# Kernel tuning notes

Measured on AMD Instinct MI355X. Metric: run time of the kernel, lower is better.

The kernel has to match this reference:

```python
import jax, jax.numpy as jnp
import numpy as np

N_NODES = 100000
N_EDGES = 3200000
FEAT = 128
HID = 128
N_GRAPHS = 512


def setup_inputs() -> dict:
    key = jax.random.key(0)
    ks = jax.random.split(key, 16)
    x = jax.random.normal(ks[0], (N_NODES, FEAT), dtype=jnp.float32)
    edge_index = jax.random.randint(ks[1], (2, N_EDGES), 0, N_NODES, dtype=jnp.int32)
    edge_weight = jax.random.uniform(ks[2], (N_EDGES,), dtype=jnp.float32)
    batch = jnp.sort(jax.random.randint(ks[3], (N_NODES,), 0, N_GRAPHS, dtype=jnp.int32))
    s = 1.0 / np.sqrt(HID)
    W1 = jax.random.uniform(ks[4], (FEAT, HID), dtype=jnp.float32, minval=-s, maxval=s)
    W2 = jax.random.uniform(ks[5], (HID, HID), dtype=jnp.float32, minval=-s, maxval=s)
    W3 = jax.random.uniform(ks[6], (HID, HID), dtype=jnp.float32, minval=-s, maxval=s)
    W4 = jax.random.uniform(ks[7], (HID, HID), dtype=jnp.float32, minval=-s, maxval=s)
    b1 = jnp.zeros((HID,), jnp.float32)
    b2 = jnp.zeros((HID,), jnp.float32)
    b3 = jnp.zeros((HID,), jnp.float32)
    b4 = jnp.zeros((HID,), jnp.float32)
    Wc = jax.random.uniform(ks[8], (HID, 1), dtype=jnp.float32, minval=-s, maxval=s)
    bc = jnp.zeros((1,), jnp.float32)
    return dict(x=x, edge_index=edge_index, edge_weight=edge_weight, batch=batch,
                W1=W1, b1=b1, W2=W2, b2=b2, W3=W3, b3=b3, W4=W4, b4=b4, Wc=Wc, bc=bc)


def _gcn_norm(edge_index, edge_weight, n):
    # PyG gcn_norm with add_self_loops=True (self-loop weight 1)
    loop = jnp.arange(n, dtype=edge_index.dtype)
    src = jnp.concatenate([edge_index[0], loop])
    dst = jnp.concatenate([edge_index[1], loop])
    ew = jnp.concatenate([edge_weight, jnp.ones((n,), edge_weight.dtype)])
    deg = jax.ops.segment_sum(ew, dst, num_segments=n)
    dinv = jnp.where(deg > 0, jax.lax.rsqrt(jnp.maximum(deg, 1e-30)), 0.0)
    norm = dinv[src] * ew * dinv[dst]
    return src, dst, norm


def _gcn_conv(x, src, dst, norm, W, b, n):
    h = x @ W                      # [N, H] dense GEMM
    msg = h[src] * norm[:, None]   # [E+N, H] gather + scale
    out = jax.ops.segment_sum(msg, dst, num_segments=n)  # scatter-add
    return out + b


def reference(x, edge_index, edge_weight, batch,
              W1, b1, W2, b2, W3, b3, W4, b4, Wc, bc):
    n = x.shape[0]
    src, dst, norm = _gcn_norm(edge_index, edge_weight, n)
    h = jax.nn.relu(_gcn_conv(x, src, dst, norm, W1, b1, n))
    h = jax.nn.relu(_gcn_conv(h, src, dst, norm, W2, b2, n))
    h = jax.nn.relu(_gcn_conv(h, src, dst, norm, W3, b3, n))
    h = jax.nn.relu(_gcn_conv(h, src, dst, norm, W4, b4, n))
    # global mean pool over graphs
    sums = jax.ops.segment_sum(h, batch, num_segments=N_GRAPHS)
    cnt = jax.ops.segment_sum(jnp.ones((n,), h.dtype), batch, num_segments=N_GRAPHS)
    pooled = sums / jnp.maximum(cnt, 1.0)[:, None]
    return jax.nn.sigmoid(pooled @ Wc + bc)
```

## Files before the change

### kernel.cpp

```cpp
#include <hip/hip_runtime.h>
#include <math.h>


#define MASK40 ((1ull << 40) - 1)

typedef float v2f __attribute__((ext_vector_type(2)));
typedef __bf16 bf16x8 __attribute__((ext_vector_type(8)));
typedef float f32x4 __attribute__((ext_vector_type(4)));

__device__ inline unsigned f2bf(float x) {
    unsigned u = __float_as_uint(x);
    return (u + 0x7FFFu + ((u >> 16) & 1u)) >> 16;
}

__global__ void init_packed(unsigned long long* packed, int n) {
    int i = blockIdx.x * blockDim.x + threadIdx.x;
    if (i < n) packed[i] = 0ull;
}

__global__ void edge_pass(const int* __restrict__ dst, const float* __restrict__ ew,
                          unsigned long long* packed, unsigned short* __restrict__ slot,
                          int E) {
    int e = blockIdx.x * blockDim.x + threadIdx.x;
    if (e < E) {
        int d = dst[e];
        unsigned int fx = (unsigned int)rintf(ew[e] * 16777216.0f);
        unsigned long long old =
            atomicAdd(&packed[d], (1ull << 40) | (unsigned long long)fx);
        slot[e] = (unsigned short)(old >> 40);
    }
}

__global__ void dinv_cnt_k(const unsigned long long* __restrict__ packed,
                           float* dinv, int* cnt, int n) {
    int i = blockIdx.x * blockDim.x + threadIdx.x;
    if (i < n) {
        unsigned long long p = packed[i];
        float deg = 1.0f + (float)(p & MASK40) * (1.0f / 16777216.0f);
        dinv[i] = rsqrtf(deg);
        cnt[i] = (int)(p >> 40);
    }
}

__global__ __launch_bounds__(1024) void scan1(const int* __restrict__ cnt, int* rowp,
                                              int* bsums, int total, int N) {
    __shared__ int sh[1024];
    int i = blockIdx.x * 1024 + threadIdx.x;
    int v = 0;
    if (i < N) v = cnt[i] + 1;
    sh[threadIdx.x] = v;
    __syncthreads();
    for (int off = 1; off < 1024; off <<= 1) {
        int t = (threadIdx.x >= (unsigned)off) ? sh[threadIdx.x - off] : 0;
        __syncthreads();
        sh[threadIdx.x] += t;
        __syncthreads();
    }
    if (i < total) rowp[i] = sh[threadIdx.x] - v;
    if (threadIdx.x == 1023) bsums[blockIdx.x] = sh[1023];
}

__global__ void scan2(int* bsums, int nb) {
    if (threadIdx.x == 0 && blockIdx.x == 0) {
        int run = 0;
        for (int b = 0; b < nb; ++b) { int t = bsums[b]; bsums[b] = run; run += t; }
    }
}

__global__ __launch_bounds__(1024) void scan3(int* rowp, const int* __restrict__ bsums,
                                              int total) {
    int i = blockIdx.x * 1024 + threadIdx.x;
    if (i < total) rowp[i] += bsums[blockIdx.x];
}

__global__ void selfloop_k(const int* __restrict__ rowp, const float* __restrict__ dinv,
                           int2* colval, int n) {
    int i = blockIdx.x * blockDim.x + threadIdx.x;
    if (i < n) {
        float dv = dinv[i];
        int2 cv;
        cv.x = i;
        cv.y = __float_as_int(dv * dv);
        colval[rowp[i]] = cv;
    }
}

__global__ void scatter2(const int* __restrict__ src, const int* __restrict__ dst,
                         const float* __restrict__ ew,
                         const unsigned short* __restrict__ slot,
                         const float* __restrict__ dinv, const int* __restrict__ rowp,
                         int2* colval, int E) {
    int e = blockIdx.x * blockDim.x + threadIdx.x;
    if (e < E) {
        int s = src[e], d = dst[e];
        int idx = rowp[d] + 1 + (int)slot[e];
        int2 cv;
        cv.x = s;
        cv.y = __float_as_int(dinv[s] * ew[e] * dinv[d]);
        colval[idx] = cv;
    }
}

__global__ void cvt_x(const float2* __restrict__ x, unsigned* __restrict__ xb,
                      long n64) {
    long t = (long)blockIdx.x * 256 + threadIdx.x;
    if (t < n64) {
        float2 f = x[t];
        xb[t] = f2bf(f.x) | (f2bf(f.y) << 16);
    }
}

__global__ void prep_w(const float* __restrict__ Wa, const float* __restrict__ Wb,
                       const float* __restrict__ Wc, const float* __restrict__ Wd,
                       unsigned short* __restrict__ Wt) {
    const int l = blockIdx.y;
    const float* W = (l == 0) ? Wa : (l == 1) ? Wb : (l == 2) ? Wc : Wd;
    const int c = blockIdx.x, p = threadIdx.x;
    int k;
    if (l == 0) {
        k = p;
    } else {
        int t = p >> 1, h = p & 1;
        int i = t >> 2, s = (t >> 1) & 1, jj = 2 * (t & 1) + h;
        k = 16 * (4 * s + jj) + i;
    }
    float v = W[k * 128 + c];
    unsigned u = __float_as_uint(v);
    Wt[l * 16384 + c * 128 + p] = (unsigned short)((u + 0x7FFFu + ((u >> 16) & 1u)) >> 16);
}

__global__ __launch_bounds__(256) void gemm_mfma(const uint4* __restrict__ A,
                                                 const uint4* __restrict__ Wt,
                                                 uint2* __restrict__ C) {
    const int w = threadIdx.x >> 6;
    const int lane = threadIdx.x & 63;
    const int i = lane & 15, q = lane >> 4;
    const long row_base = (long)blockIdx.x * 64 + w * 16;

    f32x4 acc[8];
#pragma unroll
    for (int t = 0; t < 8; ++t) acc[t] = (f32x4){0.f, 0.f, 0.f, 0.f};

    const uint4* Arow = A + (row_base + i) * 16 + q;
#pragma unroll
    for (int ks = 0; ks < 4; ++ks) {
        const bf16x8 af = __builtin_bit_cast(bf16x8, Arow[ks * 4]);
#pragma unroll
        for (int ct = 0; ct < 8; ++ct) {
            const bf16x8 bf = __builtin_bit_cast(
                bf16x8, Wt[(size_t)(ct * 16 + i) * 16 + ks * 4 + q]);
            acc[ct] = __builtin_amdgcn_mfma_f32_16x16x32_bf16(af, bf, acc[ct], 0, 0, 0);
        }
    }

#pragma unroll
    for (int reg = 0; reg < 4; ++reg) {
        int d0 = __builtin_amdgcn_cvt_pk_fp8_f32(acc[0][reg], acc[1][reg], 0, false);
        d0     = __builtin_amdgcn_cvt_pk_fp8_f32(acc[2][reg], acc[3][reg], d0, true);
        int d1 = __builtin_amdgcn_cvt_pk_fp8_f32(acc[4][reg], acc[5][reg], 0, false);
        d1     = __builtin_amdgcn_cvt_pk_fp8_f32(acc[6][reg], acc[7][reg], d1, true);
        const long row = row_base + q * 4 + reg;
        uint2 o; o.x = (unsigned)d0; o.y = (unsigned)d1;
        C[row * 16 + i] = o;
    }
}

__device__ inline int perm_f0(int lane) {
    return 64 * ((lane >> 1) & 1) + 32 * (lane & 1) + (lane >> 2);
}

__global__ __launch_bounds__(64) void aggregate(const unsigned short* __restrict__ t8,
                                                const int* __restrict__ rowp,
                                                const int2* __restrict__ colval,
                                                const float* __restrict__ bias,
                                                unsigned* __restrict__ out16, int n) {
    const int v = blockIdx.x;
    const int lane = threadIdx.x;
    const int e0 = rowp[v], e1 = rowp[v + 1];
    float ax = 0.f, ay = 0.f;
    int e = e0;
    for (; e + 4 <= e1; e += 4) {
        const int2 cv0 = colval[e],     cv1 = colval[e + 1];
        const int2 cv2 = colval[e + 2], cv3 = colval[e + 3];
        const unsigned short u0 = t8[(size_t)cv0.x * 64 + lane];
        const unsigned short u1 = t8[(size_t)cv1.x * 64 + lane];
        const unsigned short u2 = t8[(size_t)cv2.x * 64 + lane];
        const unsigned short u3 = t8[(size_t)cv3.x * 64 + lane];
        const float w0 = __int_as_float(cv0.y), w1 = __int_as_float(cv1.y);
        const float w2 = __int_as_float(cv2.y), w3 = __int_as_float(cv3.y);
        const v2f h0 = __builtin_amdgcn_cvt_pk_f32_fp8((int)u0, false);
        const v2f h1 = __builtin_amdgcn_cvt_pk_f32_fp8((int)u1, false);
        const v2f h2 = __builtin_amdgcn_cvt_pk_f32_fp8((int)u2, false);
        const v2f h3 = __builtin_amdgcn_cvt_pk_f32_fp8((int)u3, false);
        ax = fmaf(w0, h0.x, ax); ay = fmaf(w0, h0.y, ay);
        ax = fmaf(w1, h1.x, ax); ay = fmaf(w1, h1.y, ay);
        ax = fmaf(w2, h2.x, ax); ay = fmaf(w2, h2.y, ay);
        ax = fmaf(w3, h3.x, ax); ay = fmaf(w3, h3.y, ay);
    }
    for (; e < e1; ++e) {
        const int2 cv = colval[e];
        const v2f hv = __builtin_amdgcn_cvt_pk_f32_fp8(
            (int)t8[(size_t)cv.x * 64 + lane], false);
        const float w = __int_as_float(cv.y);
        ax = fmaf(w, hv.x, ax); ay = fmaf(w, hv.y, ay);
    }
    const int f0 = perm_f0(lane);
    const float rx = fmaxf(ax + bias[f0], 0.f);
    const float ry = fmaxf(ay + bias[f0 + 16], 0.f);
    out16[(size_t)v * 64 + lane] = f2bf(rx) | (f2bf(ry) << 16);
}

__global__ __launch_bounds__(64) void aggregate_last(const unsigned short* __restrict__ t8,
                                                     const int* __restrict__ rowp,
                                                     const int2* __restrict__ colval,
                                                     const float* __restrict__ bias,
                                                     const float* __restrict__ Wc,
                                                     float* __restrict__ sv, int n) {
    const int v = blockIdx.x;
    const int lane = threadIdx.x;
    const int e0 = rowp[v], e1 = rowp[v + 1];
    float ax = 0.f, ay = 0.f;
    int e = e0;
    for (; e + 4 <= e1; e += 4) {
        const int2 cv0 = colval[e],     cv1 = colval[e + 1];
        const int2 cv2 = colval[e + 2], cv3 = colval[e + 3];
        const unsigned short u0 = t8[(size_t)cv0.x * 64 + lane];
        const unsigned short u1 = t8[(size_t)cv1.x * 64 + lane];
        const unsigned short u2 = t8[(size_t)cv2.x * 64 + lane];
        const unsigned short u3 = t8[(size_t)cv3.x * 64 + lane];
        const float w0 = __int_as_float(cv0.y), w1 = __int_as_float(cv1.y);
        const float w2 = __int_as_float(cv2.y), w3 = __int_as_float(cv3.y);
        const v2f h0 = __builtin_amdgcn_cvt_pk_f32_fp8((int)u0, false);
        const v2f h1 = __builtin_amdgcn_cvt_pk_f32_fp8((int)u1, false);
        const v2f h2 = __builtin_amdgcn_cvt_pk_f32_fp8((int)u2, false);
        const v2f h3 = __builtin_amdgcn_cvt_pk_f32_fp8((int)u3, false);
        ax = fmaf(w0, h0.x, ax); ay = fmaf(w0, h0.y, ay);
        ax = fmaf(w1, h1.x, ax); ay = fmaf(w1, h1.y, ay);
        ax = fmaf(w2, h2.x, ax); ay = fmaf(w2, h2.y, ay);
        ax = fmaf(w3, h3.x, ax); ay = fmaf(w3, h3.y, ay);
    }
    for (; e < e1; ++e) {
        const int2 cv = colval[e];
        const v2f hv = __builtin_amdgcn_cvt_pk_f32_fp8(
            (int)t8[(size_t)cv.x * 64 + lane], false);
        const float w = __int_as_float(cv.y);
        ax = fmaf(w, hv.x, ax); ay = fmaf(w, hv.y, ay);
    }
    const int f0 = perm_f0(lane);
    float p = fmaxf(ax + bias[f0], 0.f) * Wc[f0] +
              fmaxf(ay + bias[f0 + 16], 0.f) * Wc[f0 + 16];
#pragma unroll
    for (int off = 32; off; off >>= 1) p += __shfl_down(p, off);
    if (lane == 0) sv[v] = p;
}

__global__ void gstart_k(const int* __restrict__ batch, int* start, int N, int G) {
    int g = blockIdx.x * blockDim.x + threadIdx.x;
    if (g <= G) {
        int lo = 0, hi = N;
        while (lo < hi) {
            int mid = (lo + hi) >> 1;
            if (batch[mid] < g) lo = mid + 1; else hi = mid;
        }
        start[g] = lo;
    }
}

__global__ __launch_bounds__(256) void seg_pool(const float* __restrict__ sv,
                                                const int* __restrict__ start,
                                                const float* __restrict__ bc,
                                                float* __restrict__ out, int G) {
    __shared__ float sh[4];
    const int g = blockIdx.x;
    const int s = start[g], epos = start[g + 1];
    float acc = 0.f;
    for (int i = s + threadIdx.x; i < epos; i += 256) acc += sv[i];
#pragma unroll
    for (int off = 32; off; off >>= 1) acc += __shfl_down(acc, off);
    if ((threadIdx.x & 63) == 0) sh[threadIdx.x >> 6] = acc;
    __syncthreads();
    if (threadIdx.x == 0) {
        float sum = sh[0] + sh[1] + sh[2] + sh[3];
        float cnt = (float)(epos - s);
        float z = sum / fmaxf(cnt, 1.0f) + bc[0];
        out[g] = 1.0f / (1.0f + expf(-z));
    }
}

extern "C" void kernel_launch(void* const* d_in, const int* in_sizes, int n_in,
                              void* d_out, int out_size, void* d_ws, size_t ws_size,
                              hipStream_t stream) {
    const float* x   = (const float*)d_in[0];
    const int* ei    = (const int*)d_in[1];
    const float* ew  = (const float*)d_in[2];
    const int* batch = (const int*)d_in[3];
    const float* W1 = (const float*)d_in[4];  const float* b1 = (const float*)d_in[5];
    const float* W2 = (const float*)d_in[6];  const float* b2 = (const float*)d_in[7];
    const float* W3 = (const float*)d_in[8];  const float* b3 = (const float*)d_in[9];
    const float* W4 = (const float*)d_in[10]; const float* b4 = (const float*)d_in[11];
    const float* Wc = (const float*)d_in[12]; const float* bc = (const float*)d_in[13];

    const int N = in_sizes[0] / 128;
    const int E = in_sizes[2];
    const int G = out_size;
    const int* src = ei;
    const int* dst = ei + E;
    const int nblk = (N + 63) / 64;
    const long Npad = (long)nblk * 64;

    char* p = (char*)d_ws;
    auto alloc = [&](size_t bytes) {
        void* q = (void*)p;
        p += (bytes + 255) & ~(size_t)255;
        return q;
    };
    unsigned long long* packed = (unsigned long long*)alloc((size_t)N * 8);
    float* dinv = (float*)alloc((size_t)N * 4);
    int* cnt    = (int*)alloc((size_t)N * 4);
    unsigned short* slot = (unsigned short*)alloc((size_t)E * 2);
    int* rowp   = (int*)alloc((size_t)(N + 1) * 4);
    int* bsums  = (int*)alloc(1024 * 4);
    const size_t M = (size_t)E + (size_t)N;
    int2* colval = (int2*)alloc(M * 8);
    unsigned* tbuf = (unsigned*)alloc((size_t)Npad * 32 * 4);
    unsigned* hbuf = (unsigned*)alloc((size_t)Npad * 64 * 4);
    unsigned* xb   = (unsigned*)alloc((size_t)Npad * 64 * 4);
    unsigned short* Wt = (unsigned short*)alloc(4 * 16384 * 2);
    float* sv   = (float*)alloc((size_t)N * 4);
    int* start  = (int*)alloc((size_t)(G + 1) * 4);

    const int B = 256;
    init_packed<<<(N + B - 1) / B, B, 0, stream>>>(packed, N);
    edge_pass<<<(E + B - 1) / B, B, 0, stream>>>(dst, ew, packed, slot, E);
    dinv_cnt_k<<<(N + B - 1) / B, B, 0, stream>>>(packed, dinv, cnt, N);
    const int total = N + 1;
    const int nb = (total + 1023) / 1024;
    scan1<<<nb, 1024, 0, stream>>>(cnt, rowp, bsums, total, N);
    scan2<<<1, 64, 0, stream>>>(bsums, nb);
    scan3<<<nb, 1024, 0, stream>>>(rowp, bsums, total);
    selfloop_k<<<(N + B - 1) / B, B, 0, stream>>>(rowp, dinv, colval, N);
    scatter2<<<(E + B - 1) / B, B, 0, stream>>>(src, dst, ew, slot, dinv, rowp,
                                                colval, E);
    gstart_k<<<(G + 1 + B - 1) / B, B, 0, stream>>>(batch, start, N, G);

    const long n64 = (long)N * 64;
    cvt_x<<<(int)((n64 + 255) / 256), B, 0, stream>>>((const float2*)x, xb, n64);
    prep_w<<<dim3(128, 4), 128, 0, stream>>>(W1, W2, W3, W4, Wt);

    const unsigned short* t8 = (const unsigned short*)tbuf;
    const uint4* Wt4 = (const uint4*)Wt;
    gemm_mfma<<<nblk, B, 0, stream>>>((const uint4*)xb,   Wt4,         (uint2*)tbuf);
    aggregate<<<N, 64, 0, stream>>>(t8, rowp, colval, b1, hbuf, N);
    gemm_mfma<<<nblk, B, 0, stream>>>((const uint4*)hbuf, Wt4 + 2048,  (uint2*)tbuf);
    aggregate<<<N, 64, 0, stream>>>(t8, rowp, colval, b2, hbuf, N);
    gemm_mfma<<<nblk, B, 0, stream>>>((const uint4*)hbuf, Wt4 + 4096,  (uint2*)tbuf);
    aggregate<<<N, 64, 0, stream>>>(t8, rowp, colval, b3, hbuf, N);
    gemm_mfma<<<nblk, B, 0, stream>>>((const uint4*)hbuf, Wt4 + 6144,  (uint2*)tbuf);
    aggregate_last<<<N, 64, 0, stream>>>(t8, rowp, colval, b4, Wc, sv, N);

    seg_pool<<<G, B, 0, stream>>>(sv, start, bc, (float*)d_out, G);
}
```

Baseline: 859.9 us.

## Quantize GEMM outputs to FP4 with per-row scale and fuse input conversion

```diff
diff --git a/kernel.cpp b/kernel.cpp
--- a/kernel.cpp
+++ b/kernel.cpp
@@ -4,13 +4,18 @@
 
 #define MASK40 ((1ull << 40) - 1)
 
-typedef float v2f __attribute__((ext_vector_type(2)));
 typedef __bf16 bf16x8 __attribute__((ext_vector_type(8)));
 typedef float f32x4 __attribute__((ext_vector_type(4)));
 
 __device__ inline unsigned f2bf(float x) {
     unsigned u = __float_as_uint(x);
     return (u + 0x7FFFu + ((u >> 16) & 1u)) >> 16;
+}
+
+__device__ inline unsigned fp4_bf16(unsigned nib) {
+    unsigned n = nib & 7u, s = (nib >> 3) << 15;
+    unsigned t10 = (n == 0) ? 0u : (0xFCu + n - (n == 1 ? 1u : 0u));
+    return (t10 << 6) | s;
 }
 
 __global__ void init_packed(unsigned long long* packed, int n) {
@@ -31,23 +36,18 @@
     }
 }
 
-__global__ void dinv_cnt_k(const unsigned long long* __restrict__ packed,
-                           float* dinv, int* cnt, int n) {
-    int i = blockIdx.x * blockDim.x + threadIdx.x;
-    if (i < n) {
-        unsigned long long p = packed[i];
-        float deg = 1.0f + (float)(p & MASK40) * (1.0f / 16777216.0f);
-        dinv[i] = rsqrtf(deg);
-        cnt[i] = (int)(p >> 40);
-    }
-}
-
-__global__ __launch_bounds__(1024) void scan1(const int* __restrict__ cnt, int* rowp,
+__global__ __launch_bounds__(1024) void scan1(const unsigned long long* __restrict__ packed,
+                                              float* __restrict__ dinv, int* rowp,
                                               int* bsums, int total, int N) {
     __shared__ int sh[1024];
     int i = blockIdx.x * 1024 + threadIdx.x;
     int v = 0;
-    if (i < N) v = cnt[i] + 1;
+    if (i < N) {
+        unsigned long long p = packed[i];
+        float deg = 1.0f + (float)(p & MASK40) * (1.0f / 16777216.0f);
+        dinv[i] = rsqrtf(deg);
+        v = (int)(p >> 40) + 1;
+    }
     sh[threadIdx.x] = v;
     __syncthreads();
     for (int off = 1; off < 1024; off <<= 1) {
@@ -101,15 +101,6 @@
     }
 }
 
-__global__ void cvt_x(const float2* __restrict__ x, unsigned* __restrict__ xb,
-                      long n64) {
-    long t = (long)blockIdx.x * 256 + threadIdx.x;
-    if (t < n64) {
-        float2 f = x[t];
-        xb[t] = f2bf(f.x) | (f2bf(f.y) << 16);
-    }
-}
-
 __global__ void prep_w(const float* __restrict__ Wa, const float* __restrict__ Wb,
                        const float* __restrict__ Wc, const float* __restrict__ Wd,
                        unsigned short* __restrict__ Wt) {
@@ -117,92 +108,127 @@
     const float* W = (l == 0) ? Wa : (l == 1) ? Wb : (l == 2) ? Wc : Wd;
     const int c = blockIdx.x, p = threadIdx.x;
     int k;
-    if (l == 0) {
-        k = p;
-    } else {
-        int t = p >> 1, h = p & 1;
-        int i = t >> 2, s = (t >> 1) & 1, jj = 2 * (t & 1) + h;
-        k = 16 * (4 * s + jj) + i;
-    }
+    if (l == 0) k = p;
+    else       k = 32 * ((p >> 1) & 3) + (p >> 3) + 16 * (p & 1);
     float v = W[k * 128 + c];
     unsigned u = __float_as_uint(v);
     Wt[l * 16384 + c * 128 + p] = (unsigned short)((u + 0x7FFFu + ((u >> 16) & 1u)) >> 16);
 }
 
-__global__ __launch_bounds__(256) void gemm_mfma(const uint4* __restrict__ A,
+template <int FP32IN>
+__global__ __launch_bounds__(256) void gemm_mfma(const void* __restrict__ Av,
                                                  const uint4* __restrict__ Wt,
-                                                 uint2* __restrict__ C) {
+                                                 unsigned* __restrict__ C4,
+                                                 float* __restrict__ sc, int N) {
     const int w = threadIdx.x >> 6;
     const int lane = threadIdx.x & 63;
-    const int i = lane & 15, q = lane >> 4;
+    const int li = lane & 15, q = lane >> 4;
     const long row_base = (long)blockIdx.x * 64 + w * 16;
+    const long arow = (row_base + li < (long)N) ? row_base + li : (long)N - 1;
 
     f32x4 acc[8];
 #pragma unroll
     for (int t = 0; t < 8; ++t) acc[t] = (f32x4){0.f, 0.f, 0.f, 0.f};
 
-    const uint4* Arow = A + (row_base + i) * 16 + q;
 #pragma unroll
     for (int ks = 0; ks < 4; ++ks) {
-        const bf16x8 af = __builtin_bit_cast(bf16x8, Arow[ks * 4]);
+        bf16x8 af;
+        if (FP32IN) {
+            const float* Ar = (const float*)Av + arow * 128 + ks * 32 + q * 8;
+            const float4 fa = *(const float4*)Ar;
+            const float4 fb = *(const float4*)(Ar + 4);
+            unsigned p0 = f2bf(fa.x) | (f2bf(fa.y) << 16);
+            unsigned p1 = f2bf(fa.z) | (f2bf(fa.w) << 16);
+            unsigned p2 = f2bf(fb.x) | (f2bf(fb.y) << 16);
+            unsigned p3 = f2bf(fb.z) | (f2bf(fb.w) << 16);
+            uint4 u; u.x = p0; u.y = p1; u.z = p2; u.w = p3;
+            af = __builtin_bit_cast(bf16x8, u);
+        } else {
+            af = __builtin_bit_cast(bf16x8,
+                ((const uint4*)Av)[arow * 16 + ks * 4 + q]);
+        }
 #pragma unroll
         for (int ct = 0; ct < 8; ++ct) {
             const bf16x8 bf = __builtin_bit_cast(
-                bf16x8, Wt[(size_t)(ct * 16 + i) * 16 + ks * 4 + q]);
+                bf16x8, Wt[(size_t)(ct * 16 + li) * 16 + ks * 4 + q]);
             acc[ct] = __builtin_amdgcn_mfma_f32_16x16x32_bf16(af, bf, acc[ct], 0, 0, 0);
         }
     }
 
 #pragma unroll
     for (int reg = 0; reg < 4; ++reg) {
-        int d0 = __builtin_amdgcn_cvt_pk_fp8_f32(acc[0][reg], acc[1][reg], 0, false);
-        d0     = __builtin_amdgcn_cvt_pk_fp8_f32(acc[2][reg], acc[3][reg], d0, true);
-        int d1 = __builtin_amdgcn_cvt_pk_fp8_f32(acc[4][reg], acc[5][reg], 0, false);
-        d1     = __builtin_amdgcn_cvt_pk_fp8_f32(acc[6][reg], acc[7][reg], d1, true);
+        float amax = 0.f;
+#pragma unroll
+        for (int ct = 0; ct < 8; ++ct) amax = fmaxf(amax, fabsf(acc[ct][reg]));
+#pragma unroll
+        for (int m = 1; m < 16; m <<= 1) amax = fmaxf(amax, __shfl_xor(amax, m));
+        const float inv = (amax > 0.f) ? 6.0f / amax : 0.f;
         const long row = row_base + q * 4 + reg;
-        uint2 o; o.x = (unsigned)d0; o.y = (unsigned)d1;
-        C[row * 16 + i] = o;
+        if (li == 0) sc[row] = amax * (1.0f / 6.0f);
+        unsigned u = 0;
+#pragma unroll
+        for (int ct = 0; ct < 8; ++ct) {
+            const float y = acc[ct][reg] * inv;
+            const float a = fabsf(y);
+            unsigned n = (unsigned)(a >= 0.25f) + (unsigned)(a >= 0.75f)
+                       + (unsigned)(a >= 1.25f) + (unsigned)(a >= 1.75f)
+                       + (unsigned)(a >= 2.5f)  + (unsigned)(a >= 3.5f)
+                       + (unsigned)(a >= 5.0f);
+            n |= (y < 0.f) ? 8u : 0u;
+            u |= n << (ct * 4);
+        }
+        C4[row * 16 + li] = u;
     }
 }
 
 __device__ inline int perm_f0(int lane) {
-    return 64 * ((lane >> 1) & 1) + 32 * (lane & 1) + (lane >> 2);
-}
-
-__global__ __launch_bounds__(64) void aggregate(const unsigned short* __restrict__ t8,
+    return 32 * (lane & 3) + (lane >> 2);
+}
+
+__global__ __launch_bounds__(64) void aggregate(const unsigned char* __restrict__ t4,
+                                                const float* __restrict__ sc,
                                                 const int* __restrict__ rowp,
                                                 const int2* __restrict__ colval,
                                                 const float* __restrict__ bias,
                                                 unsigned* __restrict__ out16, int n) {
+    __shared__ unsigned lut[256];
     const int v = blockIdx.x;
     const int lane = threadIdx.x;
+    for (int j = lane; j < 256; j += 64)
+        lut[j] = fp4_bf16(j & 15) | (fp4_bf16(j >> 4) << 16);
+    __syncthreads();
+
     const int e0 = rowp[v], e1 = rowp[v + 1];
     float ax = 0.f, ay = 0.f;
     int e = e0;
     for (; e + 4 <= e1; e += 4) {
         const int2 cv0 = colval[e],     cv1 = colval[e + 1];
         const int2 cv2 = colval[e + 2], cv3 = colval[e + 3];
-        const unsigned short u0 = t8[(size_t)cv0.x * 64 + lane];
-        const unsigned short u1 = t8[(size_t)cv1.x * 64 + lane];
-        const unsigned short u2 = t8[(size_t)cv2.x * 64 + lane];
-        const unsigned short u3 = t8[(size_t)cv3.x * 64 + lane];
-        const float w0 = __int_as_float(cv0.y), w1 = __int_as_float(cv1.y);
-        const float w2 = __int_as_float(cv2.y), w3 = __int_as_float(cv3.y);
-        const v2f h0 = __builtin_amdgcn_cvt_pk_f32_fp8((int)u0, false);
-        const v2f h1 = __builtin_amdgcn_cvt_pk_f32_fp8((int)u1, false);
-        const v2f h2 = __builtin_amdgcn_cvt_pk_f32_fp8((int)u2, false);
-        const v2f h3 = __builtin_amdgcn_cvt_pk_f32_fp8((int)u3, false);
-        ax = fmaf(w0, h0.x, ax); ay = fmaf(w0, h0.y, ay);
-        ax = fmaf(w1, h1.x, ax); ay = fmaf(w1, h1.y, ay);
-        ax = fmaf(w2, h2.x, ax); ay = fmaf(w2, h2.y, ay);
-        ax = fmaf(w3, h3.x, ax); ay = fmaf(w3, h3.y, ay);
+        const unsigned b0 = t4[(size_t)cv0.x * 64 + lane];
+        const unsigned b1 = t4[(size_t)cv1.x * 64 + lane];
+        const unsigned b2 = t4[(size_t)cv2.x * 64 + lane];
+        const unsigned b3 = t4[(size_t)cv3.x * 64 + lane];
+        const float w0 = __int_as_float(cv0.y) * sc[cv0.x];
+        const float w1 = __int_as_float(cv1.y) * sc[cv1.x];
+        const float w2 = __int_as_float(cv2.y) * sc[cv2.x];
+        const float w3 = __int_as_float(cv3.y) * sc[cv3.x];
+        const unsigned u0 = lut[b0], u1 = lut[b1], u2 = lut[b2], u3 = lut[b3];
+        ax = fmaf(w0, __uint_as_float(u0 << 16), ax);
+        ay = fmaf(w0, __uint_as_float(u0 & 0xFFFF0000u), ay);
+        ax = fmaf(w1, __uint_as_float(u1 << 16), ax);
+        ay = fmaf(w1, __uint_as_float(u1 & 0xFFFF0000u), ay);
+        ax = fmaf(w2, __uint_as_float(u2 << 16), ax);
+        ay = fmaf(w2, __uint_as_float(u2 & 0xFFFF0000u), ay);
+        ax = fmaf(w3, __uint_as_float(u3 << 16), ax);
+        ay = fmaf(w3, __uint_as_float(u3 & 0xFFFF0000u), ay);
     }
     for (; e < e1; ++e) {
         const int2 cv = colval[e];
-        const v2f hv = __builtin_amdgcn_cvt_pk_f32_fp8(
-            (int)t8[(size_t)cv.x * 64 + lane], false);
-        const float w = __int_as_float(cv.y);
-        ax = fmaf(w, hv.x, ax); ay = fmaf(w, hv.y, ay);
+        const unsigned b = t4[(size_t)cv.x * 64 + lane];
+        const float w = __int_as_float(cv.y) * sc[cv.x];
+        const unsigned u = lut[b];
+        ax = fmaf(w, __uint_as_float(u << 16), ax);
+        ay = fmaf(w, __uint_as_float(u & 0xFFFF0000u), ay);
     }
     const int f0 = perm_f0(lane);
     const float rx = fmaxf(ax + bias[f0], 0.f);
@@ -210,41 +236,51 @@
     out16[(size_t)v * 64 + lane] = f2bf(rx) | (f2bf(ry) << 16);
 }
 
-__global__ __launch_bounds__(64) void aggregate_last(const unsigned short* __restrict__ t8,
+__global__ __launch_bounds__(64) void aggregate_last(const unsigned char* __restrict__ t4,
+                                                     const float* __restrict__ sc,
                                                      const int* __restrict__ rowp,
                                                      const int2* __restrict__ colval,
                                                      const float* __restrict__ bias,
                                                      const float* __restrict__ Wc,
                                                      float* __restrict__ sv, int n) {
+    __shared__ unsigned lut[256];
     const int v = blockIdx.x;
     const int lane = threadIdx.x;
+    for (int j = lane; j < 256; j += 64)
+        lut[j] = fp4_bf16(j & 15) | (fp4_bf16(j >> 4) << 16);
+    __syncthreads();
+
     const int e0 = rowp[v], e1 = rowp[v + 1];
     float ax = 0.f, ay = 0.f;
     int e = e0;
     for (; e + 4 <= e1; e += 4) {
         const int2 cv0 = colval[e],     cv1 = colval[e + 1];
         const int2 cv2 = colval[e + 2], cv3 = colval[e + 3];
-        const unsigned short u0 = t8[(size_t)cv0.x * 64 + lane];
-        const unsigned short u1 = t8[(size_t)cv1.x * 64 + lane];
-        const unsigned short u2 = t8[(size_t)cv2.x * 64 + lane];
-        const unsigned short u3 = t8[(size_t)cv3.x * 64 + lane];
-        const float w0 = __int_as_float(cv0.y), w1 = __int_as_float(cv1.y);
-        const float w2 = __int_as_float(cv2.y), w3 = __int_as_float(cv3.y);
-        const v2f h0 = __builtin_amdgcn_cvt_pk_f32_fp8((int)u0, false);
-        const v2f h1 = __builtin_amdgcn_cvt_pk_f32_fp8((int)u1, false);
-        const v2f h2 = __builtin_amdgcn_cvt_pk_f32_fp8((int)u2, false);
-        const v2f h3 = __builtin_amdgcn_cvt_pk_f32_fp8((int)u3, false);
-        ax = fmaf(w0, h0.x, ax); ay = fmaf(w0, h0.y, ay);
-        ax = fmaf(w1, h1.x, ax); ay = fmaf(w1, h1.y, ay);
-        ax = fmaf(w2, h2.x, ax); ay = fmaf(w2, h2.y, ay);
-        ax = fmaf(w3, h3.x, ax); ay = fmaf(w3, h3.y, ay);
+        const unsigned b0 = t4[(size_t)cv0.x * 64 + lane];
+        const unsigned b1 = t4[(size_t)cv1.x * 64 + lane];
+        const unsigned b2 = t4[(size_t)cv2.x * 64 + lane];
+        const unsigned b3 = t4[(size_t)cv3.x * 64 + lane];
+        const float w0 = __int_as_float(cv0.y) * sc[cv0.x];
+        const float w1 = __int_as_float(cv1.y) * sc[cv1.x];
+        const float w2 = __int_as_float(cv2.y) * sc[cv2.x];
+        const float w3 = __int_as_float(cv3.y) * sc[cv3.x];
+        const unsigned u0 = lut[b0], u1 = lut[b1], u2 = lut[b2], u3 = lut[b3];
+        ax = fmaf(w0, __uint_as_float(u0 << 16), ax);
+        ay = fmaf(w0, __uint_as_float(u0 & 0xFFFF0000u), ay);
+        ax = fmaf(w1, __uint_as_float(u1 << 16), ax);
+        ay = fmaf(w1, __uint_as_float(u1 & 0xFFFF0000u), ay);
+        ax = fmaf(w2, __uint_as_float(u2 << 16), ax);
+        ay = fmaf(w2, __uint_as_float(u2 & 0xFFFF0000u), ay);
+        ax = fmaf(w3, __uint_as_float(u3 << 16), ax);
+        ay = fmaf(w3, __uint_as_float(u3 & 0xFFFF0000u), ay);
     }
     for (; e < e1; ++e) {
         const int2 cv = colval[e];
-        const v2f hv = __builtin_amdgcn_cvt_pk_f32_fp8(
-            (int)t8[(size_t)cv.x * 64 + lane], false);
-        const float w = __int_as_float(cv.y);
-        ax = fmaf(w, hv.x, ax); ay = fmaf(w, hv.y, ay);
+        const unsigned b = t4[(size_t)cv.x * 64 + lane];
+        const float w = __int_as_float(cv.y) * sc[cv.x];
+        const unsigned u = lut[b];
+        ax = fmaf(w, __uint_as_float(u << 16), ax);
+        ay = fmaf(w, __uint_as_float(u & 0xFFFF0000u), ay);
     }
     const int f0 = perm_f0(lane);
     float p = fmaxf(ax + bias[f0], 0.f) * Wc[f0] +
@@ -316,15 +352,14 @@
     };
     unsigned long long* packed = (unsigned long long*)alloc((size_t)N * 8);
     float* dinv = (float*)alloc((size_t)N * 4);
-    int* cnt    = (int*)alloc((size_t)N * 4);
     unsigned short* slot = (unsigned short*)alloc((size_t)E * 2);
     int* rowp   = (int*)alloc((size_t)(N + 1) * 4);
     int* bsums  = (int*)alloc(1024 * 4);
     const size_t M = (size_t)E + (size_t)N;
     int2* colval = (int2*)alloc(M * 8);
-    unsigned* tbuf = (unsigned*)alloc((size_t)Npad * 32 * 4);
+    unsigned* tbuf = (unsigned*)alloc((size_t)Npad * 16 * 4);
+    float* scb     = (float*)alloc((size_t)Npad * 4);
     unsigned* hbuf = (unsigned*)alloc((size_t)Npad * 64 * 4);
-    unsigned* xb   = (unsigned*)alloc((size_t)Npad * 64 * 4);
     unsigned short* Wt = (unsigned short*)alloc(4 * 16384 * 2);
     float* sv   = (float*)alloc((size_t)N * 4);
     int* start  = (int*)alloc((size_t)(G + 1) * 4);
@@ -332,31 +367,27 @@
     const int B = 256;
     init_packed<<<(N + B - 1) / B, B, 0, stream>>>(packed, N);
     edge_pass<<<(E + B - 1) / B, B, 0, stream>>>(dst, ew, packed, slot, E);
-    dinv_cnt_k<<<(N + B - 1) / B, B, 0, stream>>>(packed, dinv, cnt, N);
     const int total = N + 1;
     const int nb = (total + 1023) / 1024;
-    scan1<<<nb, 1024, 0, stream>>>(cnt, rowp, bsums, total, N);
+    scan1<<<nb, 1024, 0, stream>>>(packed, dinv, rowp, bsums, total, N);
     scan2<<<1, 64, 0, stream>>>(bsums, nb);
     scan3<<<nb, 1024, 0, stream>>>(rowp, bsums, total);
     selfloop_k<<<(N + B - 1) / B, B, 0, stream>>>(rowp, dinv, colval, N);
     scatter2<<<(E + B - 1) / B, B, 0, stream>>>(src, dst, ew, slot, dinv, rowp,
                                                 colval, E);
     gstart_k<<<(G + 1 + B - 1) / B, B, 0, stream>>>(batch, start, N, G);
-
-    const long n64 = (long)N * 64;
-    cvt_x<<<(int)((n64 + 255) / 256), B, 0, stream>>>((const float2*)x, xb, n64);
     prep_w<<<dim3(128, 4), 128, 0, stream>>>(W1, W2, W3, W4, Wt);
 
-    const unsigned short* t8 = (const unsigned short*)tbuf;
+    const unsigned char* t4 = (const unsigned char*)tbuf;
     const uint4* Wt4 = (const uint4*)Wt;
-    gemm_mfma<<<nblk, B, 0, stream>>>((const uint4*)xb,   Wt4,         (uint2*)tbuf);
-    aggregate<<<N, 64, 0, stream>>>(t8, rowp, colval, b1, hbuf, N);
-    gemm_mfma<<<nblk, B, 0, stream>>>((const uint4*)hbuf, Wt4 + 2048,  (uint2*)tbuf);
-    aggregate<<<N, 64, 0, stream>>>(t8, rowp, colval, b2, hbuf, N);
-    gemm_mfma<<<nblk, B, 0, stream>>>((const uint4*)hbuf, Wt4 + 4096,  (uint2*)tbuf);
-    aggregate<<<N, 64, 0, stream>>>(t8, rowp, colval, b3, hbuf, N);
-    gemm_mfma<<<nblk, B, 0, stream>>>((const uint4*)hbuf, Wt4 + 6144,  (uint2*)tbuf);
-    aggregate_last<<<N, 64, 0, stream>>>(t8, rowp, colval, b4, Wc, sv, N);
+    gemm_mfma<1><<<nblk, B, 0, stream>>>(x,    Wt4,        tbuf, scb, N);
+    aggregate<<<N, 64, 0, stream>>>(t4, scb, rowp, colval, b1, hbuf, N);
+    gemm_mfma<0><<<nblk, B, 0, stream>>>(hbuf, Wt4 + 2048, tbuf, scb, N);
+    aggregate<<<N, 64, 0, stream>>>(t4, scb, rowp, colval, b2, hbuf, N);
+    gemm_mfma<0><<<nblk, B, 0, stream>>>(hbuf, Wt4 + 4096, tbuf, scb, N);
+    aggregate<<<N, 64, 0, stream>>>(t4, scb, rowp, colval, b3, hbuf, N);
+    gemm_mfma<0><<<nblk, B, 0, stream>>>(hbuf, Wt4 + 6144, tbuf, scb, N);
+    aggregate_last<<<N, 64, 0, stream>>>(t4, scb, rowp, colval, b4, Wc, sv, N);
 
     seg_pool<<<G, B, 0, stream>>>(sv, start, bc, (float*)d_out, G);
 }
```

After: 966.2 us. 12.4% more time.
